# Optimization experiments

Hardware: AMD Instinct MI355X
Metric: run time of the kernel (lower is better)

Reference implementation:

```python
import jax, jax.numpy as jnp
import numpy as np

N_HEAD = 8


def build_mask(T, N):
    """Boolean mask [L, L], True = blocked. Mirrors the torch st_mask construction
    for text_mask_mode='part_only', text_to_motion_attn=False, all domains present."""
    L = 3 * T + 5 * N
    motion = 3 * T
    m = np.zeros((L, L), dtype=bool)
    # motion x motion: start fully blocked, then carve block-causal structure
    m[:motion, :motion] = True
    causal = np.tril(np.ones((T, T), dtype=bool))          # incl. diagonal
    strict = np.tril(np.ones((T, T), dtype=bool), k=-1)    # strictly lower
    m[0:T, 0:T] = ~causal
    m[T:2*T, 0:T] = ~causal
    m[T:2*T, T:2*T] = ~strict
    m[T:2*T, 2*T:3*T] = ~strict
    m[2*T:3*T, 0:T] = ~causal
    m[2*T:3*T, T:2*T] = ~causal
    m[2*T:3*T, 2*T:3*T] = ~strict
    # motion queries cannot see text keys
    m[:motion, motion:] = True
    # text queries cannot see motion keys (text_to_motion_attn=False)
    m[motion:, :motion] = True
    # part_only: upper-body rows see upper/torso/whole/simple_tag text domains;
    # lower-body rows see lower/torso/whole/simple_tag text domains
    ts = motion
    up, down = slice(T, 2*T), slice(2*T, 3*T)
    for d in (0, 2, 3, 4):
        m[up, ts + d*N: ts + (d+1)*N] = False
    for d in (1, 2, 3, 4):
        m[down, ts + d*N: ts + (d+1)*N] = False
    # text x text region stays all-False (full attention among text tokens)
    return jnp.asarray(m)


def setup_inputs() -> dict:
    key = jax.random.key(0)
    ks = jax.random.split(key, 9)
    B, T_motion, N, C = 2, 1024, 64, 512
    L = 3 * T_motion + 5 * N
    s = 1.0 / np.sqrt(C)
    return {
        "x": jax.random.normal(ks[0], (B, L, C), dtype=jnp.float32),
        "Wq": jax.random.normal(ks[1], (C, C), dtype=jnp.float32) * s,
        "bq": jnp.zeros((C,), dtype=jnp.float32),
        "Wk": jax.random.normal(ks[2], (C, C), dtype=jnp.float32) * s,
        "bk": jnp.zeros((C,), dtype=jnp.float32),
        "Wv": jax.random.normal(ks[3], (C, C), dtype=jnp.float32) * s,
        "bv": jnp.zeros((C,), dtype=jnp.float32),
        "Wp": jax.random.normal(ks[4], (C, C), dtype=jnp.float32) * s,
        "bp": jnp.zeros((C,), dtype=jnp.float32),
        "T_motion": T_motion,
        "N": N,
    }


def reference(x, Wq, bq, Wk, bk, Wv, bv, Wp, bp, T_motion, N):
    B, L, C = x.shape
    H = N_HEAD
    dh = C // H
    mask = build_mask(int(T_motion), int(N))  # [L, L] bool, True = blocked

    def split_heads(t):  # [B, L, C] -> [B, H, L, dh]
        return t.reshape(B, L, H, dh).transpose(0, 2, 1, 3)

    q = split_heads(x @ Wq + bq)
    k = split_heads(x @ Wk + bk)
    v = split_heads(x @ Wv + bv)

    att = jnp.einsum("bhqd,bhkd->bhqk", q, k) * (1.0 / np.sqrt(dh))
    att = jnp.where(mask[None, None], -jnp.inf, att)
    att = jax.nn.softmax(att, axis=-1)
    y = jnp.einsum("bhqk,bhkd->bhqd", att, v)
    y = y.transpose(0, 2, 1, 3).reshape(B, L, C)
    return y @ Wp + bp
```

## Files before the change

kernel.cpp:

```cpp
#include <hip/hip_runtime.h>
#include <hip/hip_bf16.h>
#include <math.h>

typedef __attribute__((ext_vector_type(8))) short bf16x8;
typedef __attribute__((ext_vector_type(4))) short short4v;
typedef __attribute__((ext_vector_type(4))) float f32x4;
typedef __attribute__((ext_vector_type(2))) unsigned int u32x2;

#define DEVI __device__ __forceinline__

constexpr int Bb  = 2;
constexpr int Tm  = 1024;
constexpr int Ntx = 64;
constexpr int Hh  = 8;
constexpr int Ll  = 3*Tm + 5*Ntx;
constexpr int Mm  = Bb*Ll;
constexpr int MOT = 3*Tm;
constexpr int UPH = 75;
constexpr int PST = 72;

DEVI short f2b(float f) {
  unsigned u = __builtin_bit_cast(unsigned, f);
  u = u + 0x7fffu + ((u >> 16) & 1u);
  return (short)(u >> 16);
}

DEVI void gld16(const void* g, void* l) {
  __builtin_amdgcn_global_load_lds(
      (const __attribute__((address_space(1))) unsigned*)g,
      (__attribute__((address_space(3))) unsigned*)l, 16, 0, 0);
}

DEVI f32x4 mfma16(bf16x8 a, bf16x8 b, f32x4 c) {
  return __builtin_amdgcn_mfma_f32_16x16x32_bf16(a, b, c, 0, 0, 0);
}


__global__ __launch_bounds__(256) void cast_x_kern(const float* __restrict__ x,
                                                   short* __restrict__ xb) {
  int i = (blockIdx.x*256 + threadIdx.x)*4;
  float4 v = *(const float4*)(x + i);
  short4v r;
  r.x = f2b(v.x); r.y = f2b(v.y); r.z = f2b(v.z); r.w = f2b(v.w);
  *(short4v*)(xb + i) = r;
}

__global__ __launch_bounds__(256) void prep_w_kern(
    const float* __restrict__ Wq, const float* __restrict__ Wk,
    const float* __restrict__ Wv, const float* __restrict__ Wp,
    short* __restrict__ WtQKV, short* __restrict__ WpT) {
  int idx = blockIdx.x*256 + threadIdx.x;
  int mat = idx >> 18;
  int n = (idx >> 9) & 511;
  int k = idx & 511;
  const float* W = (mat == 0) ? Wq : (mat == 1) ? Wk : (mat == 2) ? Wv : Wp;
  short s = f2b(W[k*512 + n]);
  if (mat < 3) WtQKV[((size_t)(mat*512 + n))*512 + k] = s;
  else         WpT[(size_t)n*512 + k] = s;
}


template<int MODE>
__global__ __launch_bounds__(256) void gemm_bt(
    const short* __restrict__ A, const short* __restrict__ Bt,
    const float* __restrict__ bias_q, const float* __restrict__ bias_k,
    const float* __restrict__ bias_v,
    short* __restrict__ Qb, short* __restrict__ Kb, short* __restrict__ Vt,
    float* __restrict__ outf) {
  __shared__ __align__(16) short At[128*32];
  __shared__ __align__(16) short Bs[128*32];
  const int tid = threadIdx.x;
  const int w = tid >> 6, lane = tid & 63;
  const int col = lane & 15, g = lane >> 4;
  const int tm = blockIdx.x, tn = blockIdx.y;
  const int wm = w >> 1, wn = w & 1;

  f32x4 acc[4][4] = {};

  for (int k0 = 0; k0 < 512; k0 += 32) {
    __syncthreads();
#pragma unroll
    for (int it = 0; it < 2; ++it) {
      int e0 = w*512 + it*2048 + lane*8;
      int row = e0 >> 5, cc = e0 & 31;
      gld16(A  + (size_t)(tm*128 + row)*512 + k0 + cc, At + w*512 + it*2048);
      gld16(Bt + (size_t)(tn*128 + row)*512 + k0 + cc, Bs + w*512 + it*2048);
    }
    __syncthreads();
    bf16x8 af[4], bfr[4];
#pragma unroll
    for (int i = 0; i < 4; ++i)
      af[i] = *(const bf16x8*)(At + (wm*64 + i*16 + col)*32 + g*8);
#pragma unroll
    for (int j = 0; j < 4; ++j)
      bfr[j] = *(const bf16x8*)(Bs + (wn*64 + j*16 + col)*32 + g*8);
#pragma unroll
    for (int i = 0; i < 4; ++i)
#pragma unroll
      for (int j = 0; j < 4; ++j)
        acc[i][j] = mfma16(af[i], bfr[j], acc[i][j]);
  }

#pragma unroll
  for (int i = 0; i < 4; ++i) {
    int mbase = tm*128 + wm*64 + i*16 + g*4;
#pragma unroll
    for (int j = 0; j < 4; ++j) {
      int ncol = tn*128 + wn*64 + j*16 + col;
#pragma unroll
      for (int r = 0; r < 4; ++r) {
        int mrow = mbase + r;
        float v = acc[i][j][r];
        if constexpr (MODE == 0) {
          float bias = (ncol < 512) ? bias_q[ncol]
                     : (ncol < 1024) ? bias_k[ncol - 512] : bias_v[ncol - 1024];
          v += bias;
          int bb = (mrow >= Ll) ? 1 : 0;
          int lpos = mrow - bb*Ll;
          int nn = ncol & 511;
          int h = nn >> 6, dd = nn & 63;
          int bh = bb*8 + h;
          if (ncol < 512) {
            Qb[((size_t)(bh*Ll + lpos))*64 + dd] = f2b(v*0.18033688f);
          } else if (ncol < 1024) {
            Kb[((size_t)(bh*Ll + lpos))*64 + dd] = f2b(v);
          } else {
            Vt[((size_t)(bh*64 + dd))*Ll + lpos] = f2b(v);
          }
        } else {
          outf[(size_t)mrow*512 + ncol] = v + bias_q[ncol];
        }
      }
    }
  }
}


__global__ __launch_bounds__(256) void attn_kern(
    const short* __restrict__ Qb, const short* __restrict__ Kb,
    const short* __restrict__ Vt, float* __restrict__ slots,
    short* __restrict__ attout) {
  __shared__ __align__(16) short Kls[2][4096];
  __shared__ __align__(16) short Vls[2][4096];
  __shared__ __align__(16) short Pls[4][32*PST];
  const int tid = threadIdx.x;
  const int w = tid >> 6, lane = tid & 63;
  const int col = lane & 15, g = lane >> 4;

  const int v  = (blockIdx.x & 7)*150 + (blockIdx.x >> 3);
  const int bh = v / UPH;
  const int lr = v - bh*UPH;

  int qsec, seg = 0, j = 0, t3 = 0;
  if (lr < 56) {
    int jj = lr/7, s = lr - jj*7;
    j = 7 - jj;
    if (s == 0)      qsec = 0;
    else if (s <= 3) { qsec = 1; seg = s - 1; }
    else             { qsec = 2; seg = s - 4; }
  } else if (lr < 72) {
    int t = lr - 56; qsec = 1 + (t & 1); j = t >> 1; seg = 3;
  } else { qsec = 3; t3 = lr - 72; }

  const int q0b = (qsec < 3) ? qsec*Tm + j*128 : MOT + ((t3 == 2) ? 192 : t3*128);
  const int t0w = j*128 + w*32;
  const int q0w = q0b + w*32;

  int kbase = 0, off = 0, nb;
  bool masked;
  if (qsec == 3)      { kbase = MOT;  nb = 5;       masked = false; }
  else if (qsec == 0) { kbase = 0;    nb = 2*j + 2; masked = true; off = 0; }
  else if (seg == 0)  { kbase = 0;    nb = 2*j + 2; masked = true; off = 0; }
  else if (seg == 1)  { kbase = Tm;   nb = 2*j + 2; masked = true; off = (qsec == 1) ? 1 : 0; }
  else if (seg == 2)  { kbase = 2*Tm; nb = 2*j + 2; masked = true; off = 1; }
  else                { kbase = 0;    nb = 4;       masked = false; }

  auto keyof = [&](int i) -> int {
    if (qsec == 3) return MOT + i*64;
    if (!masked) { int d = (i == 0) ? ((qsec == 1) ? 0 : 1) : i + 1; return MOT + d*64; }
    return kbase + i*64;
  };

  const short* Kbase_ = Kb + (size_t)bh*Ll*64;
  const short* Vbase_ = Vt + (size_t)bh*64*Ll;

  bf16x8 aq[2][2];
#pragma unroll
  for (int qf = 0; qf < 2; ++qf) {
    const short* p = Qb + ((size_t)bh*Ll + q0w + qf*16 + col)*64;
    aq[qf][0] = *(const bf16x8*)(p + g*8);
    aq[qf][1] = *(const bf16x8*)(p + 32 + g*8);
  }
  const int qv[2] = { t0w + col, t0w + 16 + col };

  float ls[2] = {0.f, 0.f};
  f32x4 out[2][4] = {};

  auto stage = [&](int buf, int key0) {
#pragma unroll
    for (int it = 0; it < 2; ++it) {
      int L = it*4096 + tid*16;
      int row = L >> 7;
      int sw = (row & 7) << 4;
      gld16((const char*)Kbase_ + (size_t)key0*128 + (L ^ sw),
            (char*)&Kls[buf][0] + it*4096 + w*1024);
      gld16((const char*)(Vbase_ + (size_t)row*Ll + key0) + ((L & 127) ^ sw),
            (char*)&Vls[buf][0] + it*4096 + w*1024);
    }
  };

  auto compute = [&](int buf, int i) {
    const int swc = (col & 7) << 4;
    f32x4 s[2][4];
#pragma unroll
    for (int kk = 0; kk < 4; ++kk) {
      const char* base = (const char*)&Kls[buf][0] + (kk*16 + col)*128;
      bf16x8 k0 = *(const bf16x8*)(base + ((g*16) ^ swc));
      bf16x8 k1 = *(const bf16x8*)(base + ((64 + g*16) ^ swc));
#pragma unroll
      for (int qf = 0; qf < 2; ++qf) {
        f32x4 t = {0,0,0,0};
        t = mfma16(k0, aq[qf][0], t);
        t = mfma16(k1, aq[qf][1], t);
        s[qf][kk] = t;
      }
    }
    const bool dm = masked && (i*64 + 63 + off > t0w);
    const int kl = i*64 + off + g*4;
    short* pw = &Pls[w][0];
#pragma unroll
    for (int qf = 0; qf < 2; ++qf) {
      float lsl = 0.f;
#pragma unroll
      for (int kk = 0; kk < 4; ++kk) {
        float pe[4];
#pragma unroll
        for (int r = 0; r < 4; ++r) {
          float p = __builtin_amdgcn_exp2f(s[qf][kk][r]);
          if (dm && (kl + kk*16 + r > qv[qf])) p = 0.f;
          pe[r] = p; lsl += p;
        }
        unsigned pk0, pk1;
        asm("v_cvt_pk_bf16_f32 %0, %1, %2" : "=v"(pk0) : "v"(pe[0]), "v"(pe[1]));
        asm("v_cvt_pk_bf16_f32 %0, %1, %2" : "=v"(pk1) : "v"(pe[2]), "v"(pe[3]));
        u32x2 pk; pk.x = pk0; pk.y = pk1;
        *(u32x2*)(pw + (qf*16 + col)*PST + kk*16 + g*4) = pk;
      }
      ls[qf] += lsl;
    }
    bf16x8 pa[2][2];
#pragma unroll
    for (int qf = 0; qf < 2; ++qf) {
      const short* base2 = &Pls[w][0] + (qf*16 + col)*PST;
      pa[qf][0] = *(const bf16x8*)(base2 + g*8);
      pa[qf][1] = *(const bf16x8*)(base2 + 32 + g*8);
    }
#pragma unroll
    for (int ch = 0; ch < 4; ++ch) {
      const char* base = (const char*)&Vls[buf][0] + (ch*16 + col)*128;
      bf16x8 v0 = *(const bf16x8*)(base + ((g*16) ^ swc));
      bf16x8 v1 = *(const bf16x8*)(base + ((64 + g*16) ^ swc));
#pragma unroll
      for (int qf = 0; qf < 2; ++qf) {
        out[qf][ch] = mfma16(pa[qf][0], v0, out[qf][ch]);
        out[qf][ch] = mfma16(pa[qf][1], v1, out[qf][ch]);
      }
    }
  };

  stage(0, keyof(0));
  for (int i = 0; i < nb; ++i) {
    if (i + 1 < nb) {
      stage((i + 1) & 1, keyof(i + 1));
      asm volatile("s_waitcnt vmcnt(4)" ::: "memory");
    } else {
      asm volatile("s_waitcnt vmcnt(0)" ::: "memory");
    }
    __builtin_amdgcn_sched_barrier(0);
    __builtin_amdgcn_s_barrier();
    bool skip = masked && (t0w + 31 < i*64 + off);
    if (!skip) compute(i & 1, i);
    __builtin_amdgcn_s_barrier();
  }

  float rs[2];
#pragma unroll
  for (int qf = 0; qf < 2; ++qf) {
    float t = ls[qf];
    t += __shfl_xor(t, 16);
    t += __shfl_xor(t, 32);
    rs[qf] = t;
  }

  if (qsec == 1 || qsec == 2) {
    float* sp = slots + ((((size_t)bh*2 + (qsec - 1))*8 + j)*4 + seg)*8320;
#pragma unroll
    for (int qf = 0; qf < 2; ++qf) {
#pragma unroll
      for (int ch = 0; ch < 4; ++ch)
#pragma unroll
        for (int r = 0; r < 4; ++r)
          sp[(w*32 + qf*16 + g*4 + r)*64 + ch*16 + col] = out[qf][ch][r];
      if (g == 0)
        sp[8192 + w*32 + qf*16 + col] = rs[qf];
    }
  } else {
    const int b = bh >> 3, h = bh & 7;
#pragma unroll
    for (int qf = 0; qf < 2; ++qf)
#pragma unroll
      for (int r = 0; r < 4; ++r) {
        float dv = __shfl(rs[qf], g*4 + r);
        float inv = 1.0f / dv;
        size_t rowoff = ((size_t)(b*Ll + q0w + qf*16 + g*4 + r))*512 + h*64;
#pragma unroll
        for (int ch = 0; ch < 4; ++ch)
          attout[rowoff + ch*16 + col] = f2b(out[qf][ch][r]*inv);
      }
  }
}

__global__ __launch_bounds__(256) void fin_kern(const float* __restrict__ slots,
                                                short* __restrict__ attout) {
  const int w = threadIdx.x >> 6, lane = threadIdx.x & 63;
  const int ridx = blockIdx.x*4 + w;
  const int bh = ridx >> 11;
  const int rr = ridx & 2047;
  const int qsec = 1 + (rr >> 10);
  const int rl = rr & 1023;
  const int j = rl >> 7;
  const int row_local = rl & 127;
  const float* base = slots + (((size_t)bh*2 + (qsec - 1))*8 + j)*4*8320;
  float a = 0.f, l = 0.f;
#pragma unroll
  for (int s = 0; s < 4; ++s) {
    a += base[s*8320 + row_local*64 + lane];
    l += base[s*8320 + 8192 + row_local];
  }
  const int b = bh >> 3, h = bh & 7;
  attout[((size_t)(b*Ll + qsec*Tm + rl))*512 + h*64 + lane] = f2b(a / l);
}


extern "C" void kernel_launch(void* const* d_in, const int* in_sizes, int n_in,
                              void* d_out, int out_size, void* d_ws, size_t ws_size,
                              hipStream_t stream) {
  const float* x  = (const float*)d_in[0];
  const float* Wq = (const float*)d_in[1];
  const float* bq = (const float*)d_in[2];
  const float* Wk = (const float*)d_in[3];
  const float* bk = (const float*)d_in[4];
  const float* Wv = (const float*)d_in[5];
  const float* bv = (const float*)d_in[6];
  const float* Wp = (const float*)d_in[7];
  const float* bp = (const float*)d_in[8];
  float* out = (float*)d_out;

  short* ws = (short*)d_ws;
  constexpr size_t SZ  = (size_t)Mm*512;
  short* xb    = ws;
  short* WtQKV = xb + SZ;
  short* WpT   = WtQKV + (size_t)1536*512;
  short* Qb    = WpT + (size_t)512*512;
  short* Kb    = Qb + SZ;
  short* Vt    = Kb + SZ;
  short* att   = Vt + SZ;
  float* slots = (float*)(att + SZ);

  cast_x_kern<<<dim3(Mm*512/1024), dim3(256), 0, stream>>>(x, xb);
  prep_w_kern<<<dim3(4096), dim3(256), 0, stream>>>(Wq, Wk, Wv, Wp, WtQKV, WpT);
  gemm_bt<0><<<dim3(53, 12), dim3(256), 0, stream>>>(xb, WtQKV, bq, bk, bv,
                                                     Qb, Kb, Vt, nullptr);
  attn_kern<<<dim3(1200), dim3(256), 0, stream>>>(Qb, Kb, Vt, slots, att);
  fin_kern<<<dim3(8192), dim3(256), 0, stream>>>(slots, att);
  gemm_bt<1><<<dim3(53, 4), dim3(256), 0, stream>>>(att, WpT, bp, nullptr, nullptr,
                                                    nullptr, nullptr, nullptr, out);
}
```

Before: 101.5 us.

## Merge prep kernels and restructure attention P buffer, V preload, priorities

The x cast and weight transpose kernels become a single launch that dispatches on block index, removing one kernel launch. In the attention kernel, the P scratch tile shrinks to one 16-row swizzled buffer per wave that is reused for each query fragment. V fragments are preloaded from shared memory before the QK MFMAs, and s_setprio is raised around the MFMA sections. Launch bounds now request 4 blocks per CU, which may limit registers and cause spills given the extra V registers held live.

```diff
diff --git a/kernel.cpp b/kernel.cpp
--- a/kernel.cpp
+++ b/kernel.cpp
@@ -17,7 +17,6 @@
 constexpr int Mm  = Bb*Ll;
 constexpr int MOT = 3*Tm;
 constexpr int UPH = 75;
-constexpr int PST = 72;
 
 DEVI short f2b(float f) {
   unsigned u = __builtin_bit_cast(unsigned, f);
@@ -36,27 +35,27 @@
 }
 
 
-__global__ __launch_bounds__(256) void cast_x_kern(const float* __restrict__ x,
-                                                   short* __restrict__ xb) {
-  int i = (blockIdx.x*256 + threadIdx.x)*4;
-  float4 v = *(const float4*)(x + i);
-  short4v r;
-  r.x = f2b(v.x); r.y = f2b(v.y); r.z = f2b(v.z); r.w = f2b(v.w);
-  *(short4v*)(xb + i) = r;
-}
-
-__global__ __launch_bounds__(256) void prep_w_kern(
+__global__ __launch_bounds__(256) void prep_kern(
+    const float* __restrict__ x,  short* __restrict__ xb,
     const float* __restrict__ Wq, const float* __restrict__ Wk,
     const float* __restrict__ Wv, const float* __restrict__ Wp,
     short* __restrict__ WtQKV, short* __restrict__ WpT) {
-  int idx = blockIdx.x*256 + threadIdx.x;
-  int mat = idx >> 18;
-  int n = (idx >> 9) & 511;
-  int k = idx & 511;
-  const float* W = (mat == 0) ? Wq : (mat == 1) ? Wk : (mat == 2) ? Wv : Wp;
-  short s = f2b(W[k*512 + n]);
-  if (mat < 3) WtQKV[((size_t)(mat*512 + n))*512 + k] = s;
-  else         WpT[(size_t)n*512 + k] = s;
+  if (blockIdx.x < 3392) {
+    int i = (blockIdx.x*256 + threadIdx.x)*4;
+    float4 v = *(const float4*)(x + i);
+    short4v r;
+    r.x = f2b(v.x); r.y = f2b(v.y); r.z = f2b(v.z); r.w = f2b(v.w);
+    *(short4v*)(xb + i) = r;
+  } else {
+    int idx = (blockIdx.x - 3392)*256 + threadIdx.x;
+    int mat = idx >> 18;
+    int n = (idx >> 9) & 511;
+    int k = idx & 511;
+    const float* W = (mat == 0) ? Wq : (mat == 1) ? Wk : (mat == 2) ? Wv : Wp;
+    short s = f2b(W[k*512 + n]);
+    if (mat < 3) WtQKV[((size_t)(mat*512 + n))*512 + k] = s;
+    else         WpT[(size_t)n*512 + k] = s;
+  }
 }
 
 
@@ -136,13 +135,13 @@
 }
 
 
-__global__ __launch_bounds__(256) void attn_kern(
+__global__ __launch_bounds__(256, 4) void attn_kern(
     const short* __restrict__ Qb, const short* __restrict__ Kb,
     const short* __restrict__ Vt, float* __restrict__ slots,
     short* __restrict__ attout) {
   __shared__ __align__(16) short Kls[2][4096];
   __shared__ __align__(16) short Vls[2][4096];
-  __shared__ __align__(16) short Pls[4][32*PST];
+  __shared__ __align__(16) short Pls[4][16*64];
   const int tid = threadIdx.x;
   const int w = tid >> 6, lane = tid & 63;
   const int col = lane & 15, g = lane >> 4;
@@ -195,6 +194,7 @@
 
   float ls[2] = {0.f, 0.f};
   f32x4 out[2][4] = {};
+  char* pwb = (char*)&Pls[w][0];
 
   auto stage = [&](int buf, int key0) {
 #pragma unroll
@@ -211,7 +211,15 @@
 
   auto compute = [&](int buf, int i) {
     const int swc = (col & 7) << 4;
+    bf16x8 vb[4][2];
+#pragma unroll
+    for (int ch = 0; ch < 4; ++ch) {
+      const char* base = (const char*)&Vls[buf][0] + (ch*16 + col)*128;
+      vb[ch][0] = *(const bf16x8*)(base + ((g*16) ^ swc));
+      vb[ch][1] = *(const bf16x8*)(base + ((64 + g*16) ^ swc));
+    }
     f32x4 s[2][4];
+    __builtin_amdgcn_s_setprio(1);
 #pragma unroll
     for (int kk = 0; kk < 4; ++kk) {
       const char* base = (const char*)&Kls[buf][0] + (kk*16 + col)*128;
@@ -225,9 +233,9 @@
         s[qf][kk] = t;
       }
     }
+    __builtin_amdgcn_s_setprio(0);
     const bool dm = masked && (i*64 + 63 + off > t0w);
     const int kl = i*64 + off + g*4;
-    short* pw = &Pls[w][0];
 #pragma unroll
     for (int qf = 0; qf < 2; ++qf) {
       float lsl = 0.f;
@@ -244,27 +252,18 @@
         asm("v_cvt_pk_bf16_f32 %0, %1, %2" : "=v"(pk0) : "v"(pe[0]), "v"(pe[1]));
         asm("v_cvt_pk_bf16_f32 %0, %1, %2" : "=v"(pk1) : "v"(pe[2]), "v"(pe[3]));
         u32x2 pk; pk.x = pk0; pk.y = pk1;
-        *(u32x2*)(pw + (qf*16 + col)*PST + kk*16 + g*4) = pk;
+        *(u32x2*)(pwb + col*128 + ((kk*32 + g*8) ^ swc)) = pk;
       }
       ls[qf] += lsl;
-    }
-    bf16x8 pa[2][2];
-#pragma unroll
-    for (int qf = 0; qf < 2; ++qf) {
-      const short* base2 = &Pls[w][0] + (qf*16 + col)*PST;
-      pa[qf][0] = *(const bf16x8*)(base2 + g*8);
-      pa[qf][1] = *(const bf16x8*)(base2 + 32 + g*8);
-    }
-#pragma unroll
-    for (int ch = 0; ch < 4; ++ch) {
-      const char* base = (const char*)&Vls[buf][0] + (ch*16 + col)*128;
-      bf16x8 v0 = *(const bf16x8*)(base + ((g*16) ^ swc));
-      bf16x8 v1 = *(const bf16x8*)(base + ((64 + g*16) ^ swc));
-#pragma unroll
-      for (int qf = 0; qf < 2; ++qf) {
-        out[qf][ch] = mfma16(pa[qf][0], v0, out[qf][ch]);
-        out[qf][ch] = mfma16(pa[qf][1], v1, out[qf][ch]);
-      }
+      bf16x8 pa0 = *(const bf16x8*)(pwb + col*128 + ((g*16) ^ swc));
+      bf16x8 pa1 = *(const bf16x8*)(pwb + col*128 + ((64 + g*16) ^ swc));
+      __builtin_amdgcn_s_setprio(1);
+#pragma unroll
+      for (int ch = 0; ch < 4; ++ch) {
+        out[qf][ch] = mfma16(pa0, vb[ch][0], out[qf][ch]);
+        out[qf][ch] = mfma16(pa1, vb[ch][1], out[qf][ch]);
+      }
+      __builtin_amdgcn_s_setprio(0);
     }
   };
 
@@ -367,8 +366,8 @@
   short* att   = Vt + SZ;
   float* slots = (float*)(att + SZ);
 
-  cast_x_kern<<<dim3(Mm*512/1024), dim3(256), 0, stream>>>(x, xb);
-  prep_w_kern<<<dim3(4096), dim3(256), 0, stream>>>(Wq, Wk, Wv, Wp, WtQKV, WpT);
+  prep_kern<<<dim3(3392 + 4096), dim3(256), 0, stream>>>(x, xb, Wq, Wk, Wv, Wp,
+                                                         WtQKV, WpT);
   gemm_bt<0><<<dim3(53, 12), dim3(256), 0, stream>>>(xb, WtQKV, bq, bk, bv,
                                                      Qb, Kb, Vt, nullptr);
   attn_kern<<<dim3(1200), dim3(256), 0, stream>>>(Qb, Kb, Vt, slots, att);
```

Result: slower. 129.2 us (+27.4%).
